# Performance work log

Measured on AMD Instinct MI355X. Metric: run time of the kernel, lower is better.

Reference implementation:

```python
import jax, jax.numpy as jnp
import numpy as np

BIT_LEN = 64
CGC = (21, 42)
GAP = 16
HID = 1024

def setup_inputs() -> dict:
    key = jax.random.key(0)
    ks = jax.random.split(key, 16)
    B, F = 2048, 4096
    s_fc1 = 0.01  # torch init: normal(0, 0.01) for Linear weights, zero bias
    inp = {
        'x_low': jax.random.normal(ks[0], (B, F), jnp.float32),
        'x_mid': jax.random.normal(ks[1], (B, F), jnp.float32),
        'x_hig': jax.random.normal(ks[2], (B, F), jnp.float32),
        # low/mid/hig MLPs: Linear(F,1024) -> ReLU -> Linear(1024,1024) -> ReLU (dropout = identity in eval)
        'low_W1': jax.random.normal(ks[3], (HID, F), jnp.float32) * s_fc1,
        'low_b1': jnp.zeros((HID,), jnp.float32),
        'low_W2': jax.random.normal(ks[4], (HID, HID), jnp.float32) * s_fc1,
        'low_b2': jnp.zeros((HID,), jnp.float32),
        'mid_W1': jax.random.normal(ks[5], (HID, F), jnp.float32) * s_fc1,
        'mid_b1': jnp.zeros((HID,), jnp.float32),
        'mid_W2': jax.random.normal(ks[6], (HID, HID), jnp.float32) * s_fc1,
        'mid_b2': jnp.zeros((HID,), jnp.float32),
        'hig_W1': jax.random.normal(ks[7], (HID, F), jnp.float32) * s_fc1,
        'hig_b1': jnp.zeros((HID,), jnp.float32),
        'hig_W2': jax.random.normal(ks[8], (HID, HID), jnp.float32) * s_fc1,
        'hig_b2': jnp.zeros((HID,), jnp.float32),
        # RNNCell (tanh) params; torch default uniform(-1/sqrt(H), 1/sqrt(H)); biases filled 0 by the module
        'W_ih': jax.random.uniform(ks[9], (HID, HID), jnp.float32, -1.0, 1.0) / np.sqrt(HID),
        'W_hh': jax.random.uniform(ks[10], (HID, HID), jnp.float32, -1.0, 1.0) / np.sqrt(HID),
        'b_ih': jnp.zeros((HID,), jnp.float32),
        'b_hh': jnp.zeros((HID,), jnp.float32),
        # actor head Linear(1024, 1)
        'W_act': jax.random.normal(ks[11], (1, HID), jnp.float32) * s_fc1,
        'b_act': jnp.zeros((1,), jnp.float32),
    }
    return inp

def _mlp(x, W1, b1, W2, b2):
    h = jax.nn.relu(x @ W1.T + b1)
    return jax.nn.relu(h @ W2.T + b2)

def _cell(x, h, W_ih, W_hh, b_ih, b_hh):
    return jnp.tanh(x @ W_ih.T + b_ih + h @ W_hh.T + b_hh)

def reference(x_low, x_mid, x_hig,
              low_W1, low_b1, low_W2, low_b2,
              mid_W1, mid_b1, mid_W2, mid_b2,
              hig_W1, hig_b1, hig_W2, hig_b2,
              W_ih, W_hh, b_ih, b_hh, W_act, b_act):
    xl = _mlp(x_low, low_W1, low_b1, low_W2, low_b2)
    xm = _mlp(x_mid, mid_W1, mid_b1, mid_W2, mid_b2)
    xh = _mlp(x_hig, hig_W1, hig_b1, hig_W2, hig_b2)
    hx = xh
    ipt = xh
    tip = 1  # static Python counter -> branch structure is compile-time constant
    probs = []
    for step in range(BIT_LEN):
        if step == CGC[0]:
            ipt = xm
            hx = _cell(ipt, hx, W_ih, W_hh, b_ih, b_hh)
            tip = 1
        elif step == CGC[1]:
            ipt = xl
            hx = _cell(ipt, hx, W_ih, W_hh, b_ih, b_hh)
            tip = 1
        elif tip % GAP == 0:
            hx = _cell(ipt, hx, W_ih, W_hh, b_ih, b_hh)
            tip = 1
        else:
            hx = _cell(hx, hx, W_ih, W_hh, b_ih, b_hh)
            tip = tip + 1
        probs.append(jax.nn.sigmoid(hx @ W_act.T + b_act))  # [B, 1]
    return jnp.stack(probs), hx  # [bit_len, B, 1], [B, 1024]
```

## Files before the change

kernel.cpp:

```cpp
#include <hip/hip_runtime.h>
#include <hip/hip_bf16.h>

typedef unsigned short u16;
typedef short bf16x8 __attribute__((ext_vector_type(8)));
typedef float floatx4 __attribute__((ext_vector_type(4)));

#define B_DIM 2048
#define F_DIM 4096
#define H_DIM 1024
#define NSTEP 64

__device__ __forceinline__ float fast_tanh(float x) {
    return 1.0f - 2.0f / (__expf(2.0f * x) + 1.0f);
}

__device__ __forceinline__ u16 f2b(float x) {
    union { float f; unsigned u; } v; v.f = x;
    unsigned r = v.u + 0x7FFFu + ((v.u >> 16) & 1u);
    return (u16)(r >> 16);
}

template<int F32>
__device__ __forceinline__ int4 ld8(const void* base, size_t elemOff) {
    if constexpr (F32) {
        const float* p = (const float*)base + elemOff;
        float4 lo = *(const float4*)p;
        float4 hi = *(const float4*)(p + 4);
        union { u16 h[8]; int4 v; } rr;
        rr.h[0] = f2b(lo.x); rr.h[1] = f2b(lo.y); rr.h[2] = f2b(lo.z); rr.h[3] = f2b(lo.w);
        rr.h[4] = f2b(hi.x); rr.h[5] = f2b(hi.y); rr.h[6] = f2b(hi.z); rr.h[7] = f2b(hi.w);
        return rr.v;
    } else {
        return *(const int4*)((const u16*)base + elemOff);
    }
}

template<int AF32, int WF32, int ACT, int OUT_F32>
__global__ __launch_bounds__(256)
void gemm64(const void* __restrict__ A0, const void* __restrict__ A1, const void* __restrict__ A2,
            const void* __restrict__ Wp0, const void* __restrict__ Wp1, const void* __restrict__ Wp2,
            const float* __restrict__ bia0, const float* __restrict__ bia1, const float* __restrict__ bia2,
            void* __restrict__ C0, void* __restrict__ C1, void* __restrict__ C2,
            const int N, const int K)
{
    constexpr int BM = 64, BN = 64, BK = 64, LS = 72;
    __shared__ u16 As[2][BM * LS];
    __shared__ u16 Bs[2][BN * LS];

    const int z = blockIdx.z;
    const void*  A     = (z == 0) ? A0 : (z == 1) ? A1 : A2;
    const void*  W     = (z == 0) ? Wp0 : (z == 1) ? Wp1 : Wp2;
    const float* bias1 = (z == 0) ? bia0 : (z == 1) ? bia1 : bia2;
    void*        Cout  = (z == 0) ? C0 : (z == 1) ? C1 : C2;

    const int tid  = threadIdx.x;
    const int wave = tid >> 6, lane = tid & 63;
    const int wm = wave >> 1, wn = wave & 1;
    const int r = lane & 15, q = lane >> 4;

    const int lin = blockIdx.y * 16 + blockIdx.x;
    const int mti = (lin & 7) | ((lin >> 7) << 3);
    const int nti = (lin >> 3) & 15;
    const int m0 = mti * BM, n0 = nti * BN;

    floatx4 acc[2][2];
    const floatx4 zf = {0.f, 0.f, 0.f, 0.f};
    #pragma unroll
    for (int a = 0; a < 2; a++)
        #pragma unroll
        for (int b = 0; b < 2; b++) acc[a][b] = zf;

    const int row0 = tid >> 3, kc = (tid & 7) << 3, row1 = row0 + 32;
    const size_t aOff0 = (size_t)(m0 + row0) * K + kc;
    const size_t aOff1 = (size_t)(m0 + row1) * K + kc;
    const size_t wOff0 = (size_t)(n0 + row0) * K + kc;
    const size_t wOff1 = (size_t)(n0 + row1) * K + kc;

    int4 av0 = ld8<AF32>(A, aOff0);
    int4 av1 = ld8<AF32>(A, aOff1);
    int4 bv0 = ld8<WF32>(W, wOff0);
    int4 bv1 = ld8<WF32>(W, wOff1);

    int p = 0;
    for (int kb = 0; kb < K; kb += BK) {
        *(int4*)&As[p][row0 * LS + kc] = av0;
        *(int4*)&As[p][row1 * LS + kc] = av1;
        *(int4*)&Bs[p][row0 * LS + kc] = bv0;
        *(int4*)&Bs[p][row1 * LS + kc] = bv1;
        __syncthreads();
        if (kb + BK < K) {
            av0 = ld8<AF32>(A, aOff0 + kb + BK);
            av1 = ld8<AF32>(A, aOff1 + kb + BK);
            bv0 = ld8<WF32>(W, wOff0 + kb + BK);
            bv1 = ld8<WF32>(W, wOff1 + kb + BK);
        }
        bf16x8 af[2][2], bfr[2][2];
        #pragma unroll
        for (int ks = 0; ks < 2; ks++)
            #pragma unroll
            for (int t = 0; t < 2; t++) {
                af[ks][t]  = *(const bf16x8*)&As[p][(wm * 32 + t * 16 + r) * LS + ks * 32 + q * 8];
                bfr[ks][t] = *(const bf16x8*)&Bs[p][(wn * 32 + t * 16 + r) * LS + ks * 32 + q * 8];
            }
        #pragma unroll
        for (int ks = 0; ks < 2; ks++)
            #pragma unroll
            for (int mt = 0; mt < 2; mt++)
                #pragma unroll
                for (int nt = 0; nt < 2; nt++)
                    acc[mt][nt] = __builtin_amdgcn_mfma_f32_16x16x32_bf16(af[ks][mt], bfr[ks][nt], acc[mt][nt], 0, 0, 0);
        p ^= 1;
    }

    #pragma unroll
    for (int mt = 0; mt < 2; mt++)
        #pragma unroll
        for (int nt = 0; nt < 2; nt++) {
            const int col  = n0 + wn * 32 + nt * 16 + r;
            const int rowb = m0 + wm * 32 + mt * 16 + q * 4;
            const float bb = bias1 ? bias1[col] : 0.f;
            #pragma unroll
            for (int i = 0; i < 4; i++) {
                float v = acc[mt][nt][i] + bb;
                if (ACT == 1) v = fmaxf(v, 0.f);
                if (OUT_F32) ((float*)Cout)[(size_t)(rowb + i) * N + col] = v;
                else ((u16*)Cout)[(size_t)(rowb + i) * N + col] = f2b(v);
            }
        }
}

template<int HAS_PRE, int LAST>
__global__ __launch_bounds__(256, 4)
void gemm_step(const u16* __restrict__ A, const u16* __restrict__ W,
               const float* __restrict__ bias, const float* __restrict__ pre,
               void* __restrict__ Cout, const float* __restrict__ Wact,
               float* __restrict__ logits)
{
    constexpr int BM = 64, BN = 64, BK = 64, LS = 72, K = H_DIM, N = H_DIM;
    __shared__ u16 As[2][BM * LS];
    __shared__ u16 Bs[2][BN * LS];

    const int tid  = threadIdx.x;
    const int wave = tid >> 6, lane = tid & 63;
    const int wm = wave >> 1, wn = wave & 1;
    const int r = lane & 15, q = lane >> 4;

    const int lin = blockIdx.y * 16 + blockIdx.x;
    const int mti = (lin & 7) | ((lin >> 7) << 3);
    const int nti = (lin >> 3) & 15;
    const int m0 = mti * BM, n0 = nti * BN;

    floatx4 acc[2][2];
    const floatx4 zf = {0.f, 0.f, 0.f, 0.f};
    acc[0][0] = zf; acc[0][1] = zf; acc[1][0] = zf; acc[1][1] = zf;

    const int row0 = tid >> 3, kc = (tid & 7) << 3, row1 = row0 + 32;
    const size_t aOff0 = (size_t)(m0 + row0) * K + kc;
    const size_t aOff1 = (size_t)(m0 + row1) * K + kc;
    const size_t wOff0 = (size_t)(n0 + row0) * K + kc;
    const size_t wOff1 = (size_t)(n0 + row1) * K + kc;

    int4 av0 = *(const int4*)(A + aOff0);
    int4 av1 = *(const int4*)(A + aOff1);
    int4 bv0 = *(const int4*)(W + wOff0);
    int4 bv1 = *(const int4*)(W + wOff1);

    int p = 0;
    for (int kb = 0; kb < K; kb += BK) {
        *(int4*)&As[p][row0 * LS + kc] = av0;
        *(int4*)&As[p][row1 * LS + kc] = av1;
        *(int4*)&Bs[p][row0 * LS + kc] = bv0;
        *(int4*)&Bs[p][row1 * LS + kc] = bv1;
        __syncthreads();
        if (kb + BK < K) {
            av0 = *(const int4*)(A + aOff0 + kb + BK);
            av1 = *(const int4*)(A + aOff1 + kb + BK);
            bv0 = *(const int4*)(W + wOff0 + kb + BK);
            bv1 = *(const int4*)(W + wOff1 + kb + BK);
        }
        bf16x8 af[2][2], bfr[2][2];
        #pragma unroll
        for (int ks = 0; ks < 2; ks++)
            #pragma unroll
            for (int t = 0; t < 2; t++) {
                af[ks][t]  = *(const bf16x8*)&As[p][(wm * 32 + t * 16 + r) * LS + ks * 32 + q * 8];
                bfr[ks][t] = *(const bf16x8*)&Bs[p][(wn * 32 + t * 16 + r) * LS + ks * 32 + q * 8];
            }
        #pragma unroll
        for (int ks = 0; ks < 2; ks++)
            #pragma unroll
            for (int mt = 0; mt < 2; mt++)
                #pragma unroll
                for (int nt = 0; nt < 2; nt++)
                    acc[mt][nt] = __builtin_amdgcn_mfma_f32_16x16x32_bf16(af[ks][mt], bfr[ks][nt], acc[mt][nt], 0, 0, 0);
        p ^= 1;
    }

    const int col0 = n0 + wn * 32 + r;
    const int col1 = col0 + 16;
    const float bb0 = bias[col0], bb1 = bias[col1];
    const float wa0 = Wact[col0], wa1 = Wact[col1];
    #pragma unroll
    for (int mt = 0; mt < 2; mt++) {
        const int rowb = m0 + wm * 32 + mt * 16 + q * 4;
        #pragma unroll
        for (int i = 0; i < 4; i++) {
            float v0 = acc[mt][0][i] + bb0;
            float v1 = acc[mt][1][i] + bb1;
            if (HAS_PRE) {
                v0 += pre[(size_t)(rowb + i) * N + col0];
                v1 += pre[(size_t)(rowb + i) * N + col1];
            }
            v0 = fast_tanh(v0);
            v1 = fast_tanh(v1);
            if (LAST) {
                ((float*)Cout)[(size_t)(rowb + i) * N + col0] = v0;
                ((float*)Cout)[(size_t)(rowb + i) * N + col1] = v1;
            } else {
                ((u16*)Cout)[(size_t)(rowb + i) * N + col0] = f2b(v0);
                ((u16*)Cout)[(size_t)(rowb + i) * N + col1] = f2b(v1);
            }
            acc[mt][0][i] = v0;
            acc[mt][1][i] = v1;
        }
    }

    __syncthreads();
    float* sc = (float*)As;
    #pragma unroll
    for (int mt = 0; mt < 2; mt++)
        #pragma unroll
        for (int i = 0; i < 4; i++) {
            float s = acc[mt][0][i] * wa0 + acc[mt][1][i] * wa1;
            s += __shfl_xor(s, 1);
            s += __shfl_xor(s, 2);
            s += __shfl_xor(s, 4);
            s += __shfl_xor(s, 8);
            if (r == 0) sc[wn * 64 + wm * 32 + mt * 16 + q * 4 + i] = s;
        }
    __syncthreads();
    if (tid < 64) {
        float s = sc[tid] + sc[64 + tid];
        atomicAdd(&logits[m0 + tid], s);
    }
}

__global__ void convert_bf16(const float* __restrict__ s0, const float* __restrict__ s1,
                             const float* __restrict__ s2,
                             u16* __restrict__ d0, u16* __restrict__ d1, u16* __restrict__ d2,
                             int n)
{
    const int z = blockIdx.z;
    const float* s = (z == 0) ? s0 : (z == 1) ? s1 : s2;
    u16* d = (z == 0) ? d0 : (z == 1) ? d1 : d2;
    int i = (blockIdx.x * 256 + threadIdx.x) * 8;
    if (i < n) {
        float4 lo = *(const float4*)(s + i);
        float4 hi = *(const float4*)(s + i + 4);
        union { u16 h[8]; int4 v; } rr;
        rr.h[0] = f2b(lo.x); rr.h[1] = f2b(lo.y); rr.h[2] = f2b(lo.z); rr.h[3] = f2b(lo.w);
        rr.h[4] = f2b(hi.x); rr.h[5] = f2b(hi.y); rr.h[6] = f2b(hi.z); rr.h[7] = f2b(hi.w);
        *(int4*)(d + i) = rr.v;
    }
}

__global__ void prep_w(const float* __restrict__ Wih, const float* __restrict__ Whh,
                       u16* __restrict__ Wsum, u16* __restrict__ Whhb, u16* __restrict__ Wihb,
                       const float* __restrict__ bih, const float* __restrict__ bhh,
                       float* __restrict__ bsum, int n) {
    int i = blockIdx.x * 256 + threadIdx.x;
    if (i < n) {
        float a = Wih[i], b = Whh[i];
        Wsum[i] = f2b(a + b);
        Whhb[i] = f2b(b);
        Wihb[i] = f2b(a);
    }
    if (i < H_DIM) bsum[i] = bih[i] + bhh[i];
}

__global__ void sigmoid_kernel(const float* __restrict__ logits, const float* __restrict__ b_act,
                               float* __restrict__ out, int n) {
    int i = blockIdx.x * 256 + threadIdx.x;
    if (i < n) {
        float zv = logits[i] + b_act[0];
        out[i] = 1.0f / (1.0f + __expf(-zv));
    }
}

extern "C" void kernel_launch(void* const* d_in, const int* in_sizes, int n_in,
                              void* d_out, int out_size, void* d_ws, size_t ws_size,
                              hipStream_t stream) {
    (void)in_sizes; (void)n_in; (void)out_size; (void)ws_size;
    const int Bn = B_DIM, F = F_DIM, H = H_DIM;

    const float* xin[3] = {(const float*)d_in[0], (const float*)d_in[1], (const float*)d_in[2]};
    const float* W1[3]  = {(const float*)d_in[3], (const float*)d_in[7], (const float*)d_in[11]};
    const float* b1[3]  = {(const float*)d_in[4], (const float*)d_in[8], (const float*)d_in[12]};
    const float* W2[3]  = {(const float*)d_in[5], (const float*)d_in[9], (const float*)d_in[13]};
    const float* b2[3]  = {(const float*)d_in[6], (const float*)d_in[10], (const float*)d_in[14]};
    const float* W_ih   = (const float*)d_in[15];
    const float* W_hh   = (const float*)d_in[16];
    const float* b_ih   = (const float*)d_in[17];
    const float* b_hh   = (const float*)d_in[18];
    const float* W_act  = (const float*)d_in[19];
    const float* b_act  = (const float*)d_in[20];

    const size_t MB = 1024 * 1024;
    char* ws = (char*)d_ws;
    u16*   xl     = (u16*)(ws + 0 * MB);
    u16*   xm     = (u16*)(ws + 4 * MB);
    u16*   xh     = (u16*)(ws + 8 * MB);
    u16*   hxB    = (u16*)(ws + 12 * MB);
    u16*   Wsum   = (u16*)(ws + 16 * MB);
    u16*   Whhb   = (u16*)(ws + 18 * MB);
    u16*   Wihb   = (u16*)(ws + 20 * MB);
    u16*   h1a    = (u16*)(ws + 22 * MB);
    u16*   h1b    = (u16*)(ws + 26 * MB);
    u16*   h1c    = (u16*)(ws + 30 * MB);
    u16*   Wtmp   = (u16*)(ws + 34 * MB);
    float* pre_xh = (float*)(ws + 22 * MB);
    float* pre_xm = (float*)(ws + 30 * MB);
    float* pre_xl = (float*)(ws + 38 * MB);
    float* logits = (float*)(ws + 46 * MB);
    float* bsum   = (float*)(ws + 46 * MB + 512 * 1024);

    dim3 blk(256);
    dim3 gridH(16, 32, 1);
    dim3 grid3(16, 32, 3);

    (void)hipMemsetAsync(logits, 0, (size_t)NSTEP * Bn * sizeof(float), stream);
    prep_w<<<dim3((H * H + 255) / 256), blk, 0, stream>>>(W_ih, W_hh, Wsum, Whhb, Wihb,
                                                          b_ih, b_hh, bsum, H * H);

    u16* h1[3] = {h1a, h1b, h1c};
    const int nW1 = H * F;
    for (int m = 0; m < 3; m++) {
        convert_bf16<<<dim3((nW1 / 8 + 255) / 256, 1, 1), blk, 0, stream>>>(
            W1[m], nullptr, nullptr, Wtmp, nullptr, nullptr, nW1);
        gemm64<1,0,1,0><<<gridH, blk, 0, stream>>>(
            xin[m], nullptr, nullptr, Wtmp, nullptr, nullptr, b1[m], nullptr, nullptr,
            h1[m], nullptr, nullptr, H, F);
    }
    const int nW2 = H * H;
    u16* W2b[3] = {Wtmp, Wtmp + nW2, Wtmp + 2 * nW2};
    convert_bf16<<<dim3((nW2 / 8 + 255) / 256, 1, 3), blk, 0, stream>>>(
        W2[0], W2[1], W2[2], W2b[0], W2b[1], W2b[2], nW2);
    gemm64<0,0,1,0><<<grid3, blk, 0, stream>>>(
        h1a, h1b, h1c, W2b[0], W2b[1], W2b[2], b2[0], b2[1], b2[2],
        xl, xm, xh, H, H);
    gemm64<0,0,0,1><<<grid3, blk, 0, stream>>>(
        xh, xm, xl, Wihb, Wihb, Wihb, b_ih, b_ih, b_ih,
        pre_xh, pre_xm, pre_xl, H, H);

    u16* hx = xh;
    u16* nxt = hxB;
    for (int step = 0; step < NSTEP; step++) {
        const float* pre = nullptr;
        if (step == 15) pre = pre_xh;
        else if (step == 21 || step == 37) pre = pre_xm;
        else if (step == 42 || step == 58) pre = pre_xl;
        float* lg = logits + (size_t)step * Bn;
        if (step == NSTEP - 1) {
            float* outf = (float*)d_out + (size_t)NSTEP * Bn;
            gemm_step<0,1><<<gridH, blk, 0, stream>>>(hx, Wsum, bsum, nullptr, outf, W_act, lg);
        } else if (pre) {
            gemm_step<1,0><<<gridH, blk, 0, stream>>>(hx, Whhb, b_hh, pre, nxt, W_act, lg);
        } else {
            gemm_step<0,0><<<gridH, blk, 0, stream>>>(hx, Wsum, bsum, nullptr, nxt, W_act, lg);
        }
        u16* t = hx; hx = nxt; nxt = t;
    }
    sigmoid_kernel<<<dim3((NSTEP * Bn + 255) / 256), blk, 0, stream>>>(
        logits, b_act, (float*)d_out, NSTEP * Bn);
}
```

Measured before the change: 1.333 ms.

## Widen step GEMM K-tile with XOR-swizzled LDS and fuse weight conversion into MLP GEMMs

The recurrent step GEMM moves from BK=64 with padded LDS rows to BK=128 with an XOR-swizzled unpadded layout, so there are half as many K iterations and barriers. The occupancy hint in its launch bounds is dropped. The three MLP first-layer GEMMs are batched into one grid launch that reads fp32 weights directly and converts them while loading, removing the separate convert kernels and their scratch buffer. f2b now uses the HIP bf16 intrinsic; the larger LDS footprint may cut occupancy, and in-GEMM conversion repeats the fp32 weight reads across tiles.

```diff
diff --git a/kernel.cpp b/kernel.cpp
--- a/kernel.cpp
+++ b/kernel.cpp
@@ -15,9 +15,9 @@
 }
 
 __device__ __forceinline__ u16 f2b(float x) {
-    union { float f; unsigned u; } v; v.f = x;
-    unsigned r = v.u + 0x7FFFu + ((v.u >> 16) & 1u);
-    return (u16)(r >> 16);
+    union { __hip_bfloat16 b; u16 u; } v;
+    v.b = __float2bfloat16(x);
+    return v.u;
 }
 
 template<int F32>
@@ -130,15 +130,15 @@
 }
 
 template<int HAS_PRE, int LAST>
-__global__ __launch_bounds__(256, 4)
+__global__ __launch_bounds__(256)
 void gemm_step(const u16* __restrict__ A, const u16* __restrict__ W,
                const float* __restrict__ bias, const float* __restrict__ pre,
                void* __restrict__ Cout, const float* __restrict__ Wact,
                float* __restrict__ logits)
 {
-    constexpr int BM = 64, BN = 64, BK = 64, LS = 72, K = H_DIM, N = H_DIM;
-    __shared__ u16 As[2][BM * LS];
-    __shared__ u16 Bs[2][BN * LS];
+    constexpr int BM = 64, BN = 64, BK = 128, K = H_DIM, N = H_DIM;
+    __shared__ u16 As[2][BM * BK];
+    __shared__ u16 Bs[2][BN * BK];
 
     const int tid  = threadIdx.x;
     const int wave = tid >> 6, lane = tid & 63;
@@ -154,45 +154,49 @@
     const floatx4 zf = {0.f, 0.f, 0.f, 0.f};
     acc[0][0] = zf; acc[0][1] = zf; acc[1][0] = zf; acc[1][1] = zf;
 
-    const int row0 = tid >> 3, kc = (tid & 7) << 3, row1 = row0 + 32;
-    const size_t aOff0 = (size_t)(m0 + row0) * K + kc;
-    const size_t aOff1 = (size_t)(m0 + row1) * K + kc;
-    const size_t wOff0 = (size_t)(n0 + row0) * K + kc;
-    const size_t wOff1 = (size_t)(n0 + row1) * K + kc;
-
-    int4 av0 = *(const int4*)(A + aOff0);
-    int4 av1 = *(const int4*)(A + aOff1);
-    int4 bv0 = *(const int4*)(W + wOff0);
-    int4 bv1 = *(const int4*)(W + wOff1);
-
+    const int row = tid >> 2, c = tid & 3;
+    const size_t aOff = (size_t)(m0 + row) * K + c * 8;
+    const size_t wOff = (size_t)(n0 + row) * K + c * 8;
+    int dst[4];
+    #pragma unroll
+    for (int j = 0; j < 4; j++)
+        dst[j] = row * BK + (((c * 8) + j * 32) ^ ((row & 7) * 8));
+
+    int4 av[4], bv[4];
+    #pragma unroll
+    for (int j = 0; j < 4; j++) {
+        av[j] = *(const int4*)(A + aOff + j * 32);
+        bv[j] = *(const int4*)(W + wOff + j * 32);
+    }
+
+    const int sw = (r & 7) * 8;
     int p = 0;
     for (int kb = 0; kb < K; kb += BK) {
-        *(int4*)&As[p][row0 * LS + kc] = av0;
-        *(int4*)&As[p][row1 * LS + kc] = av1;
-        *(int4*)&Bs[p][row0 * LS + kc] = bv0;
-        *(int4*)&Bs[p][row1 * LS + kc] = bv1;
+        #pragma unroll
+        for (int j = 0; j < 4; j++) {
+            *(int4*)&As[p][dst[j]] = av[j];
+            *(int4*)&Bs[p][dst[j]] = bv[j];
+        }
         __syncthreads();
         if (kb + BK < K) {
-            av0 = *(const int4*)(A + aOff0 + kb + BK);
-            av1 = *(const int4*)(A + aOff1 + kb + BK);
-            bv0 = *(const int4*)(W + wOff0 + kb + BK);
-            bv1 = *(const int4*)(W + wOff1 + kb + BK);
-        }
-        bf16x8 af[2][2], bfr[2][2];
-        #pragma unroll
-        for (int ks = 0; ks < 2; ks++)
             #pragma unroll
-            for (int t = 0; t < 2; t++) {
-                af[ks][t]  = *(const bf16x8*)&As[p][(wm * 32 + t * 16 + r) * LS + ks * 32 + q * 8];
-                bfr[ks][t] = *(const bf16x8*)&Bs[p][(wn * 32 + t * 16 + r) * LS + ks * 32 + q * 8];
-            }
-        #pragma unroll
-        for (int ks = 0; ks < 2; ks++)
-            #pragma unroll
-            for (int mt = 0; mt < 2; mt++)
-                #pragma unroll
-                for (int nt = 0; nt < 2; nt++)
-                    acc[mt][nt] = __builtin_amdgcn_mfma_f32_16x16x32_bf16(af[ks][mt], bfr[ks][nt], acc[mt][nt], 0, 0, 0);
+            for (int j = 0; j < 4; j++) {
+                av[j] = *(const int4*)(A + aOff + kb + BK + j * 32);
+                bv[j] = *(const int4*)(W + wOff + kb + BK + j * 32);
+            }
+        }
+        #pragma unroll
+        for (int ks = 0; ks < 4; ks++) {
+            const int cb = ((ks * 32) + q * 8) ^ sw;
+            bf16x8 a0 = *(const bf16x8*)&As[p][(wm * 32 +      r) * BK + cb];
+            bf16x8 a1 = *(const bf16x8*)&As[p][(wm * 32 + 16 + r) * BK + cb];
+            bf16x8 b0 = *(const bf16x8*)&Bs[p][(wn * 32 +      r) * BK + cb];
+            bf16x8 b1 = *(const bf16x8*)&Bs[p][(wn * 32 + 16 + r) * BK + cb];
+            acc[0][0] = __builtin_amdgcn_mfma_f32_16x16x32_bf16(a0, b0, acc[0][0], 0, 0, 0);
+            acc[0][1] = __builtin_amdgcn_mfma_f32_16x16x32_bf16(a0, b1, acc[0][1], 0, 0, 0);
+            acc[1][0] = __builtin_amdgcn_mfma_f32_16x16x32_bf16(a1, b0, acc[1][0], 0, 0, 0);
+            acc[1][1] = __builtin_amdgcn_mfma_f32_16x16x32_bf16(a1, b1, acc[1][1], 0, 0, 0);
+        }
         p ^= 1;
     }
 
@@ -242,25 +246,6 @@
     if (tid < 64) {
         float s = sc[tid] + sc[64 + tid];
         atomicAdd(&logits[m0 + tid], s);
-    }
-}
-
-__global__ void convert_bf16(const float* __restrict__ s0, const float* __restrict__ s1,
-                             const float* __restrict__ s2,
-                             u16* __restrict__ d0, u16* __restrict__ d1, u16* __restrict__ d2,
-                             int n)
-{
-    const int z = blockIdx.z;
-    const float* s = (z == 0) ? s0 : (z == 1) ? s1 : s2;
-    u16* d = (z == 0) ? d0 : (z == 1) ? d1 : d2;
-    int i = (blockIdx.x * 256 + threadIdx.x) * 8;
-    if (i < n) {
-        float4 lo = *(const float4*)(s + i);
-        float4 hi = *(const float4*)(s + i + 4);
-        union { u16 h[8]; int4 v; } rr;
-        rr.h[0] = f2b(lo.x); rr.h[1] = f2b(lo.y); rr.h[2] = f2b(lo.z); rr.h[3] = f2b(lo.w);
-        rr.h[4] = f2b(hi.x); rr.h[5] = f2b(hi.y); rr.h[6] = f2b(hi.z); rr.h[7] = f2b(hi.w);
-        *(int4*)(d + i) = rr.v;
     }
 }
 
@@ -317,7 +302,6 @@
     u16*   h1a    = (u16*)(ws + 22 * MB);
     u16*   h1b    = (u16*)(ws + 26 * MB);
     u16*   h1c    = (u16*)(ws + 30 * MB);
-    u16*   Wtmp   = (u16*)(ws + 34 * MB);
     float* pre_xh = (float*)(ws + 22 * MB);
     float* pre_xm = (float*)(ws + 30 * MB);
     float* pre_xl = (float*)(ws + 38 * MB);
@@ -333,20 +317,11 @@
                                                           b_ih, b_hh, bsum, H * H);
 
     u16* h1[3] = {h1a, h1b, h1c};
-    const int nW1 = H * F;
-    for (int m = 0; m < 3; m++) {
-        convert_bf16<<<dim3((nW1 / 8 + 255) / 256, 1, 1), blk, 0, stream>>>(
-            W1[m], nullptr, nullptr, Wtmp, nullptr, nullptr, nW1);
-        gemm64<1,0,1,0><<<gridH, blk, 0, stream>>>(
-            xin[m], nullptr, nullptr, Wtmp, nullptr, nullptr, b1[m], nullptr, nullptr,
-            h1[m], nullptr, nullptr, H, F);
-    }
-    const int nW2 = H * H;
-    u16* W2b[3] = {Wtmp, Wtmp + nW2, Wtmp + 2 * nW2};
-    convert_bf16<<<dim3((nW2 / 8 + 255) / 256, 1, 3), blk, 0, stream>>>(
-        W2[0], W2[1], W2[2], W2b[0], W2b[1], W2b[2], nW2);
-    gemm64<0,0,1,0><<<grid3, blk, 0, stream>>>(
-        h1a, h1b, h1c, W2b[0], W2b[1], W2b[2], b2[0], b2[1], b2[2],
+    gemm64<1,1,1,0><<<grid3, blk, 0, stream>>>(
+        xin[0], xin[1], xin[2], W1[0], W1[1], W1[2], b1[0], b1[1], b1[2],
+        h1[0], h1[1], h1[2], H, F);
+    gemm64<0,1,1,0><<<grid3, blk, 0, stream>>>(
+        h1a, h1b, h1c, W2[0], W2[1], W2[2], b2[0], b2[1], b2[2],
         xl, xm, xh, H, H);
     gemm64<0,0,0,1><<<grid3, blk, 0, stream>>>(
         xh, xm, xl, Wihb, Wihb, Wihb, b_ih, b_ih, b_ih,
```

New measurement: 1.226 ms. 8.0% less time.
